# Kernel optimization log

Hardware: AMD Instinct MI355X
Metric: run time of the kernel (lower is better)

Reference implementation:

```python
import jax, jax.numpy as jnp
import numpy as np

B, LQ, LK = 4, 2048, 2048
DQ, DK, DO = 1024, 1024, 1024


def setup_inputs() -> dict:
    key = jax.random.key(0)
    ks = jax.random.split(key, 9)
    s = 0.02
    return {
        "query_input": jax.random.normal(ks[0], (B, LQ, DQ), jnp.float32),
        "key_input": jax.random.normal(ks[1], (B, LK, DK), jnp.float32),
        "value_input": jax.random.normal(ks[2], (B, LK, DK), jnp.float32),
        "Wq": jax.random.normal(ks[3], (DQ, DO), jnp.float32) * s,
        "bq": jax.random.normal(ks[4], (DO,), jnp.float32) * s,
        "Wk": jax.random.normal(ks[5], (DK, DO), jnp.float32) * s,
        "bk": jax.random.normal(ks[6], (DO,), jnp.float32) * s,
        "Wv": jax.random.normal(ks[7], (DK, DO), jnp.float32) * s,
        "bv": jax.random.normal(ks[8], (DO,), jnp.float32) * s,
    }


def reference(query_input, key_input, value_input, Wq, bq, Wk, bk, Wv, bv):
    scale = jnp.asarray(DO, query_input.dtype) ** 0.5
    q = query_input @ Wq + bq              # [B, Lq, D]
    k = key_input @ Wk + bk                # [B, Lk, D]
    v = value_input @ Wv + bv              # [B, Lk, D]
    attn = jnp.einsum("bqd,bkd->bqk", q, k) / scale
    attn = jax.nn.softmax(attn, axis=-1)
    return jnp.einsum("bqk,bkd->bqd", attn, v)
```

## Files before the change

### kernel.cpp

```cpp
#include <hip/hip_runtime.h>

typedef _Float16 f16x8 __attribute__((ext_vector_type(8)));
typedef _Float16 f16x4 __attribute__((ext_vector_type(4)));
typedef float f32x4 __attribute__((ext_vector_type(4)));

__device__ __forceinline__ void lds_load16(const _Float16* g, _Float16* l) {
    __builtin_amdgcn_global_load_lds(
        (const __attribute__((address_space(1))) void*)g,
        (__attribute__((address_space(3))) void*)l,
        16, 0, 0);
}

template <int MODE>
__global__ __launch_bounds__(256, 2)
void gemm_nt(const _Float16* A, const _Float16* B, void* Cv, const float* bias,
             const _Float16* A2, const _Float16* B2, const float* bias2, void* C2,
             float* rowsum,
             int M, int N, int K, int lda, int ldb, int ldc,
             long long strideA, long long strideB, long long strideC, float alpha)
{
    const int z = blockIdx.z;
    size_t cbase = 0;
    if (MODE == 1) {
        if (z) { A = A2; B = B2; bias = bias2; Cv = C2; }
    } else if (MODE == 3) {
        A += (size_t)z * strideA;
        B += (size_t)z * strideB;
        cbase = (size_t)z * strideC;
        rowsum += (size_t)z * M;
    } else if (MODE == 4) {
        const int b = z >> 1, kc = z & 1;
        A += (size_t)b * strideA + (size_t)kc * 1024;
        B += (size_t)b * 2048 + (size_t)kc * 1024;
        cbase = (size_t)b * strideC;
        rowsum += (size_t)b * M;
    }

    const int m0 = blockIdx.y * 128;
    const int n0 = blockIdx.x * 128;

    __shared__ __align__(16) _Float16 As[128 * 32];
    __shared__ __align__(16) _Float16 Bs[128 * 32];

    const int t    = threadIdx.x;
    const int w    = t >> 6;
    const int lane = t & 63;
    const int ln   = lane & 15;
    const int kq   = lane >> 4;
    const int wm   = (w & 1) * 64;
    const int wn   = (w >> 1) * 64;

    const int arow = t >> 2;
    const int kcf  = (t & 3) * 8;
    const _Float16* gA0 = A + (size_t)(m0 + arow) * lda + kcf;
    const _Float16* gA1 = A + (size_t)(m0 + 64 + arow) * lda + kcf;
    const _Float16* gB0 = B + (size_t)(n0 + arow) * ldb + kcf;
    const _Float16* gB1 = B + (size_t)(n0 + 64 + arow) * ldb + kcf;
    _Float16* lA0 = As + w * 512;
    _Float16* lA1 = As + 2048 + w * 512;
    _Float16* lB0 = Bs + w * 512;
    _Float16* lB1 = Bs + 2048 + w * 512;

    f32x4 acc[4][4] = {};

    for (int k0 = 0; k0 < K; k0 += 32) {
        __syncthreads();
        lds_load16(gA0 + k0, lA0);
        lds_load16(gA1 + k0, lA1);
        lds_load16(gB0 + k0, lB0);
        lds_load16(gB1 + k0, lB1);
        __syncthreads();

        f16x8 af[4], bf[4];
#pragma unroll
        for (int i = 0; i < 4; ++i)
            af[i] = *(const f16x8*)(As + (wm + i * 16 + ln) * 32 + kq * 8);
#pragma unroll
        for (int i = 0; i < 4; ++i)
            bf[i] = *(const f16x8*)(Bs + (wn + i * 16 + ln) * 32 + kq * 8);
#pragma unroll
        for (int i = 0; i < 4; ++i)
#pragma unroll
            for (int j = 0; j < 4; ++j)
                acc[i][j] = __builtin_amdgcn_mfma_f32_16x16x32_f16(af[i], bf[j], acc[i][j], 0, 0, 0);
    }

    float*    Cf = (float*)Cv;
    _Float16* Ch = (_Float16*)Cv;
#pragma unroll
    for (int i = 0; i < 4; ++i) {
        const int rbase = m0 + wm + i * 16 + kq * 4;

        if (MODE == 1 || MODE == 2) {
#pragma unroll
            for (int j = 0; j < 4; ++j) {
                const int gcol = n0 + wn + j * 16 + ln;
#pragma unroll
                for (int r = 0; r < 4; ++r) {
                    float vv = acc[i][j][r];
                    if (MODE == 1) vv += bias[gcol];
                    if (MODE == 2) vv += bias[rbase + r];
                    Ch[cbase + (size_t)(rbase + r) * ldc + gcol] = (_Float16)vv;
                }
            }
        } else if (MODE == 3) {
            float rs[4] = {0.f, 0.f, 0.f, 0.f};
#pragma unroll
            for (int j = 0; j < 4; ++j) {
                const int gcol = n0 + wn + j * 16 + ln;
#pragma unroll
                for (int r = 0; r < 4; ++r) {
                    float e = __expf(acc[i][j][r] * alpha);
                    Ch[cbase + (size_t)(rbase + r) * ldc + gcol] = (_Float16)e;
                    rs[r] += e;
                }
            }
#pragma unroll
            for (int r = 0; r < 4; ++r) {
                float s = rs[r];
                s += __shfl_xor(s, 1);
                s += __shfl_xor(s, 2);
                s += __shfl_xor(s, 4);
                s += __shfl_xor(s, 8);
                if (ln == 0) atomicAdd(&rowsum[rbase + r], s);
            }
        } else if (MODE == 4) {
            float inv[4];
#pragma unroll
            for (int r = 0; r < 4; ++r) inv[r] = 1.f / rowsum[rbase + r];
#pragma unroll
            for (int j = 0; j < 4; ++j) {
                const int gcol = n0 + wn + j * 16 + ln;
#pragma unroll
                for (int r = 0; r < 4; ++r)
                    atomicAdd(&Cf[cbase + (size_t)(rbase + r) * ldc + gcol],
                              acc[i][j][r] * inv[r]);
            }
        }
    }
}

__global__ __launch_bounds__(256)
void cvt_and_zero(const float4* __restrict__ x0, _Float16* __restrict__ y0,
                  const float4* __restrict__ x1, _Float16* __restrict__ y1,
                  const float4* __restrict__ x2, _Float16* __restrict__ y2,
                  float* __restrict__ rowsum, float4* __restrict__ outz)
{
    const size_t i = (size_t)blockIdx.x * 256 + threadIdx.x;
    const float4* x = blockIdx.y == 0 ? x0 : blockIdx.y == 1 ? x1 : x2;
    _Float16*    yy = blockIdx.y == 0 ? y0 : blockIdx.y == 1 ? y1 : y2;
    float4 f = x[i];
    f16x4 o = { (_Float16)f.x, (_Float16)f.y, (_Float16)f.z, (_Float16)f.w };
    *(f16x4*)(yy + i * 4) = o;
    if (blockIdx.y == 0 && blockIdx.x < 32)
        rowsum[blockIdx.x * 256 + threadIdx.x] = 0.f;
    if (blockIdx.y == 1)
        outz[i] = make_float4(0.f, 0.f, 0.f, 0.f);
}

__global__ __launch_bounds__(256)
void transpose_w_1024(const float* __restrict__ W0, _Float16* __restrict__ T0,
                      const float* __restrict__ W1, _Float16* __restrict__ T1,
                      const float* __restrict__ W2, _Float16* __restrict__ T2)
{
    const float* W = blockIdx.z == 0 ? W0 : blockIdx.z == 1 ? W1 : W2;
    _Float16*   WT = blockIdx.z == 0 ? T0 : blockIdx.z == 1 ? T1 : T2;
    __shared__ float tile[32][33];
    const int bx = blockIdx.x * 32;
    const int by = blockIdx.y * 32;
    const int tx = threadIdx.x;
    const int ty = threadIdx.y;
#pragma unroll
    for (int i = ty; i < 32; i += 8)
        tile[i][tx] = W[(size_t)(by + i) * 1024 + bx + tx];
    __syncthreads();
#pragma unroll
    for (int i = ty; i < 32; i += 8)
        WT[(size_t)(bx + i) * 1024 + by + tx] = (_Float16)tile[tx][i];
}

extern "C" void kernel_launch(void* const* d_in, const int* in_sizes, int n_in,
                              void* d_out, int out_size, void* d_ws, size_t ws_size,
                              hipStream_t stream)
{
    const float* Xq = (const float*)d_in[0];
    const float* Xk = (const float*)d_in[1];
    const float* Xv = (const float*)d_in[2];
    const float* Wq = (const float*)d_in[3];
    const float* bq = (const float*)d_in[4];
    const float* Wk = (const float*)d_in[5];
    const float* bk = (const float*)d_in[6];
    const float* Wv = (const float*)d_in[7];
    const float* bv = (const float*)d_in[8];
    float* out = (float*)d_out;

    const size_t XN = (size_t)8192 * 1024;
    const size_t WN = (size_t)1024 * 1024;

    _Float16* ws  = (_Float16*)d_ws;
    _Float16* Xqh = ws;
    _Float16* Xkh = Xqh + XN;
    _Float16* Xvh = Xkh + XN;
    _Float16* WqT = Xvh + XN;
    _Float16* WkT = WqT + WN;
    _Float16* WvT = WkT + WN;
    _Float16* qh  = WvT + WN;
    _Float16* kh  = qh + XN;
    _Float16* vT  = kh + XN;
    _Float16* S   = vT + XN;
    float* rowsum = (float*)(S + (size_t)4 * 2048 * 2048);

    {
        dim3 g(8192, 3);
        cvt_and_zero<<<g, 256, 0, stream>>>((const float4*)Xq, Xqh,
                                            (const float4*)Xk, Xkh,
                                            (const float4*)Xv, Xvh,
                                            rowsum, (float4*)out);
    }

    {
        dim3 tb(32, 8), tg(32, 32, 3);
        transpose_w_1024<<<tg, tb, 0, stream>>>(Wq, WqT, Wk, WkT, Wv, WvT);
    }

    {
        dim3 g(8, 64, 2);
        gemm_nt<1><<<g, 256, 0, stream>>>(Xqh, WqT, qh, bq,
            Xkh, WkT, bk, kh, nullptr,
            8192, 1024, 1024, 1024, 1024, 1024, 0, 0, 0, 1.f);
    }
    {
        dim3 g(64, 8, 1);
        gemm_nt<2><<<g, 256, 0, stream>>>(WvT, Xvh, vT, bv,
            nullptr, nullptr, nullptr, nullptr, nullptr,
            1024, 8192, 1024, 1024, 1024, 8192, 0, 0, 0, 1.f);
    }

    {
        dim3 g(16, 16, 4);
        gemm_nt<3><<<g, 256, 0, stream>>>(qh, kh, S, nullptr,
            nullptr, nullptr, nullptr, nullptr, rowsum,
            2048, 2048, 1024, 1024, 1024, 2048,
            (long long)2048 * 1024, (long long)2048 * 1024, (long long)2048 * 2048,
            0.03125f);
    }

    {
        dim3 g(8, 16, 8);
        gemm_nt<4><<<g, 256, 0, stream>>>(S, vT, out, nullptr,
            nullptr, nullptr, nullptr, nullptr, rowsum,
            2048, 1024, 1024, 2048, 8192, 1024,
            (long long)2048 * 2048, 0, (long long)2048 * 1024,
            1.f);
    }
}
```

Baseline: 371.7 us.

## Merge QKV projection launches and drop split-K atomics in PV GEMM

Q, K and V projections now run in one 3-slice launch, with the V slice computing the transposed output by swapping block indices. The PV GEMM no longer splits K into two chunks accumulated with float atomicAdd. Each block now runs the full K=2048 and writes plain stores, so zeroing the output buffer is no longer needed. Shapes and strides are now compile-time constants. In exchange the PV grid is halved (512 blocks, each with a longer K loop), which may reduce parallelism.

```diff
diff --git a/kernel.cpp b/kernel.cpp
--- a/kernel.cpp
+++ b/kernel.cpp
@@ -13,31 +13,35 @@
 
 template <int MODE>
 __global__ __launch_bounds__(256, 2)
-void gemm_nt(const _Float16* A, const _Float16* B, void* Cv, const float* bias,
-             const _Float16* A2, const _Float16* B2, const float* bias2, void* C2,
-             float* rowsum,
-             int M, int N, int K, int lda, int ldb, int ldc,
-             long long strideA, long long strideB, long long strideC, float alpha)
+void gemm_core(const _Float16* A, const _Float16* B, void* Cv, const float* bias,
+               const _Float16* Ax1, const _Float16* Bx1, void* Cx1, const float* bx1,
+               const _Float16* Ax2, const _Float16* Bx2, void* Cx2, const float* bx2,
+               float* rowsum)
 {
     const int z = blockIdx.z;
     size_t cbase = 0;
-    if (MODE == 1) {
-        if (z) { A = A2; B = B2; bias = bias2; Cv = C2; }
+    int lda, ldb, K, m0, n0;
+    if (MODE == 0) {
+        if (z == 1) { A = Ax1; B = Bx1; Cv = Cx1; bias = bx1; }
+        else if (z == 2) { A = Ax2; B = Bx2; Cv = Cx2; bias = bx2; }
+        lda = 1024; ldb = 1024; K = 1024;
+        m0 = (z == 2 ? blockIdx.x : blockIdx.y) * 128;
+        n0 = (z == 2 ? blockIdx.y : blockIdx.x) * 128;
     } else if (MODE == 3) {
-        A += (size_t)z * strideA;
-        B += (size_t)z * strideB;
-        cbase = (size_t)z * strideC;
-        rowsum += (size_t)z * M;
-    } else if (MODE == 4) {
-        const int b = z >> 1, kc = z & 1;
-        A += (size_t)b * strideA + (size_t)kc * 1024;
-        B += (size_t)b * 2048 + (size_t)kc * 1024;
-        cbase = (size_t)b * strideC;
-        rowsum += (size_t)b * M;
-    }
-
-    const int m0 = blockIdx.y * 128;
-    const int n0 = blockIdx.x * 128;
+        A += (size_t)z * 2048 * 1024;
+        B += (size_t)z * 2048 * 1024;
+        cbase = (size_t)z * 2048 * 2048;
+        rowsum += z * 2048;
+        lda = 1024; ldb = 1024; K = 1024;
+        m0 = blockIdx.y * 128; n0 = blockIdx.x * 128;
+    } else {
+        A += (size_t)z * 2048 * 2048;
+        B += (size_t)z * 2048;
+        cbase = (size_t)z * 2048 * 1024;
+        rowsum += z * 2048;
+        lda = 2048; ldb = 8192; K = 2048;
+        m0 = blockIdx.y * 128; n0 = blockIdx.x * 128;
+    }
 
     __shared__ __align__(16) _Float16 As[128 * 32];
     __shared__ __align__(16) _Float16 Bs[128 * 32];
@@ -85,22 +89,22 @@
                 acc[i][j] = __builtin_amdgcn_mfma_f32_16x16x32_f16(af[i], bf[j], acc[i][j], 0, 0, 0);
     }
 
+    const int ldc = (MODE == 0) ? (z == 2 ? 8192 : 1024)
+                  : (MODE == 3) ? 2048 : 1024;
     float*    Cf = (float*)Cv;
     _Float16* Ch = (_Float16*)Cv;
 #pragma unroll
     for (int i = 0; i < 4; ++i) {
         const int rbase = m0 + wm + i * 16 + kq * 4;
 
-        if (MODE == 1 || MODE == 2) {
+        if (MODE == 0) {
 #pragma unroll
             for (int j = 0; j < 4; ++j) {
                 const int gcol = n0 + wn + j * 16 + ln;
 #pragma unroll
                 for (int r = 0; r < 4; ++r) {
-                    float vv = acc[i][j][r];
-                    if (MODE == 1) vv += bias[gcol];
-                    if (MODE == 2) vv += bias[rbase + r];
-                    Ch[cbase + (size_t)(rbase + r) * ldc + gcol] = (_Float16)vv;
+                    float vv = acc[i][j][r] + (z == 2 ? bias[rbase + r] : bias[gcol]);
+                    Ch[(size_t)(rbase + r) * ldc + gcol] = (_Float16)vv;
                 }
             }
         } else if (MODE == 3) {
@@ -110,7 +114,7 @@
                 const int gcol = n0 + wn + j * 16 + ln;
 #pragma unroll
                 for (int r = 0; r < 4; ++r) {
-                    float e = __expf(acc[i][j][r] * alpha);
+                    float e = __expf(acc[i][j][r] * 0.03125f);
                     Ch[cbase + (size_t)(rbase + r) * ldc + gcol] = (_Float16)e;
                     rs[r] += e;
                 }
@@ -124,7 +128,7 @@
                 s += __shfl_xor(s, 8);
                 if (ln == 0) atomicAdd(&rowsum[rbase + r], s);
             }
-        } else if (MODE == 4) {
+        } else {
             float inv[4];
 #pragma unroll
             for (int r = 0; r < 4; ++r) inv[r] = 1.f / rowsum[rbase + r];
@@ -133,18 +137,17 @@
                 const int gcol = n0 + wn + j * 16 + ln;
 #pragma unroll
                 for (int r = 0; r < 4; ++r)
-                    atomicAdd(&Cf[cbase + (size_t)(rbase + r) * ldc + gcol],
-                              acc[i][j][r] * inv[r]);
+                    Cf[cbase + (size_t)(rbase + r) * ldc + gcol] = acc[i][j][r] * inv[r];
             }
         }
     }
 }
 
 __global__ __launch_bounds__(256)
-void cvt_and_zero(const float4* __restrict__ x0, _Float16* __restrict__ y0,
-                  const float4* __restrict__ x1, _Float16* __restrict__ y1,
-                  const float4* __restrict__ x2, _Float16* __restrict__ y2,
-                  float* __restrict__ rowsum, float4* __restrict__ outz)
+void cvt_f16(const float4* __restrict__ x0, _Float16* __restrict__ y0,
+             const float4* __restrict__ x1, _Float16* __restrict__ y1,
+             const float4* __restrict__ x2, _Float16* __restrict__ y2,
+             float* __restrict__ rowsum)
 {
     const size_t i = (size_t)blockIdx.x * 256 + threadIdx.x;
     const float4* x = blockIdx.y == 0 ? x0 : blockIdx.y == 1 ? x1 : x2;
@@ -154,8 +157,6 @@
     *(f16x4*)(yy + i * 4) = o;
     if (blockIdx.y == 0 && blockIdx.x < 32)
         rowsum[blockIdx.x * 256 + threadIdx.x] = 0.f;
-    if (blockIdx.y == 1)
-        outz[i] = make_float4(0.f, 0.f, 0.f, 0.f);
 }
 
 __global__ __launch_bounds__(256)
@@ -212,10 +213,9 @@
 
     {
         dim3 g(8192, 3);
-        cvt_and_zero<<<g, 256, 0, stream>>>((const float4*)Xq, Xqh,
-                                            (const float4*)Xk, Xkh,
-                                            (const float4*)Xv, Xvh,
-                                            rowsum, (float4*)out);
+        cvt_f16<<<g, 256, 0, stream>>>((const float4*)Xq, Xqh,
+                                       (const float4*)Xk, Xkh,
+                                       (const float4*)Xv, Xvh, rowsum);
     }
 
     {
@@ -224,33 +224,29 @@
     }
 
     {
-        dim3 g(8, 64, 2);
-        gemm_nt<1><<<g, 256, 0, stream>>>(Xqh, WqT, qh, bq,
-            Xkh, WkT, bk, kh, nullptr,
-            8192, 1024, 1024, 1024, 1024, 1024, 0, 0, 0, 1.f);
-    }
-    {
-        dim3 g(64, 8, 1);
-        gemm_nt<2><<<g, 256, 0, stream>>>(WvT, Xvh, vT, bv,
-            nullptr, nullptr, nullptr, nullptr, nullptr,
-            1024, 8192, 1024, 1024, 1024, 8192, 0, 0, 0, 1.f);
+        dim3 g(8, 64, 3);
+        gemm_core<0><<<g, 256, 0, stream>>>(
+            Xqh, WqT, qh, bq,
+            Xkh, WkT, kh, bk,
+            WvT, Xvh, vT, bv,
+            nullptr);
     }
 
     {
         dim3 g(16, 16, 4);
-        gemm_nt<3><<<g, 256, 0, stream>>>(qh, kh, S, nullptr,
-            nullptr, nullptr, nullptr, nullptr, rowsum,
-            2048, 2048, 1024, 1024, 1024, 2048,
-            (long long)2048 * 1024, (long long)2048 * 1024, (long long)2048 * 2048,
-            0.03125f);
-    }
-
-    {
-        dim3 g(8, 16, 8);
-        gemm_nt<4><<<g, 256, 0, stream>>>(S, vT, out, nullptr,
-            nullptr, nullptr, nullptr, nullptr, rowsum,
-            2048, 1024, 1024, 2048, 8192, 1024,
-            (long long)2048 * 2048, 0, (long long)2048 * 1024,
-            1.f);
-    }
-}
+        gemm_core<3><<<g, 256, 0, stream>>>(
+            qh, kh, S, nullptr,
+            nullptr, nullptr, nullptr, nullptr,
+            nullptr, nullptr, nullptr, nullptr,
+            rowsum);
+    }
+
+    {
+        dim3 g(8, 16, 4);
+        gemm_core<5><<<g, 256, 0, stream>>>(
+            S, vT, out, nullptr,
+            nullptr, nullptr, nullptr, nullptr,
+            nullptr, nullptr, nullptr, nullptr,
+            rowsum);
+    }
+}
```

Result: faster. 342.3 us (-7.9%).
